# Optimization experiments

Hardware: AMD Instinct MI355X
Metric: run time of the kernel (lower is better)

The kernel has to match this reference:

```python
import jax, jax.numpy as jnp
import numpy as np

# CLIP ViT-B/16 + CLIP4Clip pruning controller dims
B, L, C = 128, 197, 768      # batch, vision tokens (CLS at 0), vis_dim
Lt, Ct = 32, 512             # text length, txt_dim
H = 12                       # n_head
DH = C // H                  # head dim = 64
DPP = 256                    # dpp_vproj output dim
TAU = 1.0                    # gumbel tau (>= 0.05 clamp is inactive)
TARGET = 0.7                 # keep_ratio for this layer
DPP_TAU = 0.01               # default dpp_tau
DPP_EPS = 1e-05


def setup_inputs() -> dict:
    key = jax.random.key(0)
    ks = jax.random.split(key, 14)
    s = 0.02
    f32 = jnp.float32
    return {
        "x_LND": jax.random.normal(ks[0], (L, B, C), f32),
        "text_hidden_BLC": jax.random.normal(ks[1], (B, Lt, Ct), f32),
        "gumbel_u": jax.random.uniform(ks[2], (B, L - 1, 2), f32),
        # q/k/v projections (torch Linear convention: W is [out, in])
        "Wq": jax.random.normal(ks[3], (C, C), f32) * s,
        "bq": jnp.zeros((C,), f32),
        "Wk": jax.random.normal(ks[4], (C, Ct), f32) * s,
        "bk": jnp.zeros((C,), f32),
        "Wv": jax.random.normal(ks[5], (C, Ct), f32) * s,
        "bv": jnp.zeros((C,), f32),
        # out_mlp: Linear(C,C) -> QuickGELU -> Linear(C,2)
        "W1": jax.random.normal(ks[6], (C, C), f32) * s,
        "b1": jnp.zeros((C,), f32),
        "W2": jax.random.normal(ks[7], (2, C), f32) * s,
        "b2": jnp.zeros((2,), f32),
        # dpp_vproj (no bias)
        "Wdpp": jax.random.normal(ks[8], (DPP, C), f32) * s,
    }


def reference(x_LND, text_hidden_BLC, gumbel_u, Wq, bq, Wk, bk, Wv, bv,
              W1, b1, W2, b2, Wdpp):
    Nv = L - 1
    # ---- LVDecisionModule: cross-attn policy head ----
    vis_all = jnp.transpose(x_LND, (1, 0, 2))      # [B, L, C]
    vis_tok = vis_all[:, 1:, :]                    # [B, Nv, C] (exclude CLS)
    q = (vis_tok @ Wq.T + bq).reshape(B, Nv, H, DH)
    k = (text_hidden_BLC @ Wk.T + bk).reshape(B, Lt, H, DH)
    v = (text_hidden_BLC @ Wv.T + bv).reshape(B, Lt, H, DH)
    scores = jnp.einsum('bnhd,blhd->bhnl', q, k) / (DH ** 0.5)  # [B,H,Nv,Lt]
    attn = jax.nn.softmax(scores, axis=-1)
    ctx = jnp.einsum('bhnl,blhd->bnhd', attn, v).reshape(B, Nv, C)
    fused = ctx + vis_tok                          # inner_dim == vis_dim
    hmid = fused @ W1.T + b1
    hmid = hmid * jax.nn.sigmoid(1.702 * hmid)     # QuickGELU
    logits = hmid @ W2.T + b2                      # [B, Nv, 2]
    rel_BN = attn.mean(axis=-1).mean(axis=1)       # [B, Nv]

    # ---- Gumbel-softmax sample ----
    eps_g = 1e-06
    U = jnp.clip(gumbel_u, eps_g, 1.0 - eps_g)
    g = -jnp.log(-jnp.log(U))
    lg = logits - jnp.max(logits, axis=-1, keepdims=True)
    probs = jax.nn.softmax((lg + g) / TAU, axis=-1)  # [B, Nv, 2]

    # ---- straight-through hard sample ----
    idx = jnp.argmax(probs, axis=-1)
    hard = jax.nn.one_hot(idx, 2, dtype=probs.dtype) + probs - jax.lax.stop_gradient(probs)
    keep_prob = probs[..., 1]                      # [B, Nv]
    keep_bin = hard[..., 1]

    # ---- ratio loss + cumulative policy (cum_policy was None) ----
    loss_ratio = (keep_prob.mean() - TARGET) ** 2
    policy = jnp.concatenate([jnp.ones((B, 1), keep_bin.dtype), keep_bin], axis=1)  # [B, L]

    # ---- DPP loss from attention relevance ----
    eps = 1e-12
    rel = jnp.maximum(rel_BN, 0.0)
    rel = rel / (rel.mean(axis=1, keepdims=True) + eps)   # quality_power == 1
    kp = jnp.clip(keep_prob, 0.0, 1.0)                    # keepprob_power == 1
    w = rel * kp
    w = jnp.maximum(w / (w.mean(axis=1, keepdims=True) + eps), 1e-06)
    w = jnp.sqrt(w)[..., None]                            # [B, Nv, 1]
    phi = vis_tok @ Wdpp.T                                # [B, Nv, DPP]
    phi = phi / jnp.maximum(jnp.linalg.norm(phi, axis=-1, keepdims=True), 1e-12)
    pw = phi * w
    G = jnp.einsum('bnd,bmd->bnm', pw, pw) / (float(DPP) * float(Nv) * DPP_TAU)
    # A = G + I, then safe_logdet adds DPP_EPS * I
    A = G + (1.0 + DPP_EPS) * jnp.eye(Nv, dtype=G.dtype)
    Lc = jnp.linalg.cholesky(A)
    logdet = 2.0 * jnp.sum(jnp.log(jnp.diagonal(Lc, axis1=-2, axis2=-1)), axis=-1)
    loss_dpp = -logdet.mean()

    return policy, loss_ratio, loss_dpp
```

## Files before the change

### kernel.cpp

```cpp
#include <hip/hip_runtime.h>
#include <math.h>

#define B_   128
#define L_   197
#define C_   768
#define Nv_  196
#define Lt_  32
#define Ct_  512
#define H_   12
#define DH_  64
#define DPP_ 256
#define MTOK 25088
#define MLD_ 208

typedef __attribute__((ext_vector_type(8))) short bf16x8_t;
typedef __attribute__((ext_vector_type(4))) float f32x4_t;

__device__ __forceinline__ void gload_lds16(const short* g, short* l) {
    __builtin_amdgcn_global_load_lds(
        (const __attribute__((address_space(1))) unsigned int*)g,
        (__attribute__((address_space(3))) unsigned int*)l,
        16, 0, 0);
}

__device__ __forceinline__ void split_bf16(float a, unsigned &h, unsigned &l) {
    unsigned u = __float_as_uint(a);
    unsigned hu = u & 0xffff0000u;
    h = hu >> 16;
    float lf = a - __uint_as_float(hu);
    unsigned ul = __float_as_uint(lf);
    l = (ul + 0x7fffu + ((ul >> 16) & 1u)) >> 16;
}

__device__ __forceinline__ void split8_pack(const float* av, uint4& Hh, uint4& Ll) {
    unsigned hv[8], lv[8];
#pragma unroll
    for (int j = 0; j < 8; ++j) split_bf16(av[j], hv[j], lv[j]);
    Hh.x = hv[0] | (hv[1] << 16); Hh.y = hv[2] | (hv[3] << 16);
    Hh.z = hv[4] | (hv[5] << 16); Hh.w = hv[6] | (hv[7] << 16);
    Ll.x = lv[0] | (lv[1] << 16); Ll.y = lv[2] | (lv[3] << 16);
    Ll.z = lv[4] | (lv[5] << 16); Ll.w = lv[6] | (lv[7] << 16);
}

#define NWQ 589824
#define NWK 393216
#define NWD 196608
__global__ __launch_bounds__(256)
void split_all(const float* __restrict__ Wq, const float* __restrict__ W1,
               const float* __restrict__ Wk, const float* __restrict__ Wv,
               const float* __restrict__ Wd,
               short* __restrict__ Wq_h, short* __restrict__ Wq_l,
               short* __restrict__ W1_h, short* __restrict__ W1_l,
               short* __restrict__ Wk_h, short* __restrict__ Wk_l,
               short* __restrict__ Wv_h, short* __restrict__ Wv_l,
               short* __restrict__ Wd_h, short* __restrict__ Wd_l)
{
    int j = blockIdx.x * 256 + threadIdx.x;
    const float* src; short *hi, *lo;
    if (j < NWQ)                { src = Wq; hi = Wq_h; lo = Wq_l; }
    else if ((j -= NWQ) < NWQ)  { src = W1; hi = W1_h; lo = W1_l; }
    else if ((j -= NWQ) < NWK)  { src = Wk; hi = Wk_h; lo = Wk_l; }
    else if ((j -= NWK) < NWK)  { src = Wv; hi = Wv_h; lo = Wv_l; }
    else                        { j -= NWK;  src = Wd; hi = Wd_h; lo = Wd_l; }
    unsigned h, l;
    split_bf16(src[j], h, l);
    hi[j] = (short)h; lo[j] = (short)l;
}

__global__ __launch_bounds__(256)
void split_x(const float* __restrict__ x, short* __restrict__ Xh,
             short* __restrict__ Xl)
{
    int idx = blockIdx.x * 256 + threadIdx.x;
    int m = idx / 96, c8 = (idx - m * 96) * 8;
    int b = m / Nv_, n = m - b * Nv_;
    const float* src = x + ((size_t)(n + 1) * B_ + b) * C_ + c8;
    float av[8];
    *(float4*)&av[0] = *(const float4*)src;
    *(float4*)&av[4] = *(const float4*)(src + 4);
    uint4 Hh, Ll;
    split8_pack(av, Hh, Ll);
    *(uint4*)&Xh[(size_t)m * C_ + c8] = Hh;
    *(uint4*)&Xl[(size_t)m * C_ + c8] = Ll;
}

__global__ __launch_bounds__(256)
void split_text(const float* __restrict__ t, short* __restrict__ Th,
                short* __restrict__ Tl)
{
    int idx = blockIdx.x * 256 + threadIdx.x;
    const float* src = t + (size_t)idx * 8;
    float av[8];
    *(float4*)&av[0] = *(const float4*)src;
    *(float4*)&av[4] = *(const float4*)(src + 4);
    uint4 Hh, Ll;
    split8_pack(av, Hh, Ll);
    *(uint4*)&Th[(size_t)idx * 8] = Hh;
    *(uint4*)&Tl[(size_t)idx * 8] = Ll;
}

template<int EPI, int SELY, int SWZ>
__global__ __launch_bounds__(256)
void mfma_gemm(const short* __restrict__ Ah_g, const short* __restrict__ Al_g,
               const short* __restrict__ Bh1, const short* __restrict__ Bl1,
               const float* __restrict__ bias1, float* __restrict__ C1, int Nst1,
               const short* Bh2, const short* Bl2, const float* bias2,
               float* C2, int Nst2,
               int Kd, const float* __restrict__ W2, float* __restrict__ partials)
{
    int bx = blockIdx.x, by = blockIdx.y;
    if (SWZ) {
        const int NX = gridDim.x, NY = gridDim.y;
        const int total = NX * NY;
        int flat = by * NX + bx;
        int g = (flat & 7) * (total >> 3) + (flat >> 3);
        bx = g / NY; by = g % NY;
    }
    const bool sel = SELY ? (by >= 6) : (blockIdx.z != 0);
    const short* Bh_g = sel ? Bh2 : Bh1;
    const short* Bl_g = sel ? Bl2 : Bl1;
    const float* bias = sel ? bias2 : bias1;
    float* Cst        = sel ? C2 : C1;
    const int Nst     = sel ? Nst2 : Nst1;
    const int yy      = (SELY && sel) ? by - 6 : by;

    __shared__ short Ah[128 * 32], Al[128 * 32], Bh[128 * 32], Bl[128 * 32];
    const int tid = threadIdx.x;
    const int m0 = bx * 128, n0 = yy * 128;
    const int l = tid & 63, wid = tid >> 6;
    const int wr = wid >> 1, wc = wid & 1;
    const int lr = l & 15, lq = l >> 4;

    const int sr = wid * 32 + (l >> 2);
    const int sc = 8 * ((l & 3) ^ ((l >> 3) & 3));
    const short* a0  = Ah_g + (size_t)(m0 + sr) * Kd + sc;
    const short* a1  = Ah_g + (size_t)(m0 + sr + 16) * Kd + sc;
    const short* al0 = Al_g + (size_t)(m0 + sr) * Kd + sc;
    const short* al1 = Al_g + (size_t)(m0 + sr + 16) * Kd + sc;
    const short* b0  = Bh_g + (size_t)(n0 + sr) * Kd + sc;
    const short* b1  = Bh_g + (size_t)(n0 + sr + 16) * Kd + sc;
    const short* bl0 = Bl_g + (size_t)(n0 + sr) * Kd + sc;
    const short* bl1 = Bl_g + (size_t)(n0 + sr + 16) * Kd + sc;
    short* dA0  = &Ah[(wid * 32) * 32];
    short* dA1  = &Ah[(wid * 32 + 16) * 32];
    short* dAl0 = &Al[(wid * 32) * 32];
    short* dAl1 = &Al[(wid * 32 + 16) * 32];
    short* dB0  = &Bh[(wid * 32) * 32];
    short* dB1  = &Bh[(wid * 32 + 16) * 32];
    short* dBl0 = &Bl[(wid * 32) * 32];
    short* dBl1 = &Bl[(wid * 32 + 16) * 32];

    const int swzr = (lr >> 1) & 3;

    f32x4_t acc[4][4];
#pragma unroll
    for (int m = 0; m < 4; ++m)
#pragma unroll
        for (int n = 0; n < 4; ++n) {
            acc[m][n][0] = 0.f; acc[m][n][1] = 0.f;
            acc[m][n][2] = 0.f; acc[m][n][3] = 0.f;
        }

    for (int k0 = 0; k0 < Kd; k0 += 32) {
        gload_lds16(a0  + k0, dA0);
        gload_lds16(a1  + k0, dA1);
        gload_lds16(al0 + k0, dAl0);
        gload_lds16(al1 + k0, dAl1);
        gload_lds16(b0  + k0, dB0);
        gload_lds16(b1  + k0, dB1);
        gload_lds16(bl0 + k0, dBl0);
        gload_lds16(bl1 + k0, dBl1);
        __syncthreads();

        bf16x8_t ahf[4], alf[4], bhf[4], blf[4];
#pragma unroll
        for (int m = 0; m < 4; ++m) {
            int ro = (wr * 64 + m * 16 + lr) * 32 + ((lq ^ swzr) * 8);
            ahf[m] = *(const bf16x8_t*)&Ah[ro];
            alf[m] = *(const bf16x8_t*)&Al[ro];
        }
#pragma unroll
        for (int n = 0; n < 4; ++n) {
            int ro = (wc * 64 + n * 16 + lr) * 32 + ((lq ^ swzr) * 8);
            bhf[n] = *(const bf16x8_t*)&Bh[ro];
            blf[n] = *(const bf16x8_t*)&Bl[ro];
        }
#pragma unroll
        for (int m = 0; m < 4; ++m)
#pragma unroll
            for (int n = 0; n < 4; ++n) {
                acc[m][n] = __builtin_amdgcn_mfma_f32_16x16x32_bf16(ahf[m], bhf[n], acc[m][n], 0, 0, 0);
                acc[m][n] = __builtin_amdgcn_mfma_f32_16x16x32_bf16(ahf[m], blf[n], acc[m][n], 0, 0, 0);
                acc[m][n] = __builtin_amdgcn_mfma_f32_16x16x32_bf16(alf[m], bhf[n], acc[m][n], 0, 0, 0);
            }
        __syncthreads();
    }

    if constexpr (EPI == 0) {
#pragma unroll
        for (int n = 0; n < 4; ++n) {
            int col = n0 + wc * 64 + n * 16 + lr;
            float bv = bias ? bias[col] : 0.f;
#pragma unroll
            for (int m = 0; m < 4; ++m) {
                int rowb = m0 + wr * 64 + m * 16 + lq * 4;
#pragma unroll
                for (int r = 0; r < 4; ++r)
                    Cst[(size_t)(rowb + r) * Nst + col] = acc[m][n][r] + bv;
            }
        }
    } else {
        int coln[4]; float b1v[4], w20[4], w21[4];
#pragma unroll
        for (int n = 0; n < 4; ++n) {
            coln[n] = n0 + wc * 64 + n * 16 + lr;
            b1v[n] = bias[coln[n]];
            w20[n] = W2[coln[n]];
            w21[n] = W2[C_ + coln[n]];
        }
        const int pi = (yy * 2 + wc) * 2;
#pragma unroll
        for (int m = 0; m < 4; ++m)
#pragma unroll
            for (int r = 0; r < 4; ++r) {
                float p0 = 0.f, p1 = 0.f;
#pragma unroll
                for (int n = 0; n < 4; ++n) {
                    float h = acc[m][n][r] + b1v[n];
                    float gl = h / (1.f + expf(-1.702f * h));
                    p0 = fmaf(gl, w20[n], p0);
                    p1 = fmaf(gl, w21[n], p1);
                }
#pragma unroll
                for (int off = 8; off; off >>= 1) {
                    p0 += __shfl_xor(p0, off, 16);
                    p1 += __shfl_xor(p1, off, 16);
                }
                if (lr == 0) {
                    int row = m0 + wr * 64 + m * 16 + lq * 4 + r;
                    partials[(size_t)row * 24 + pi + 0] = p0;
                    partials[(size_t)row * 24 + pi + 1] = p1;
                }
            }
    }
}

__global__ __launch_bounds__(256)
void gram_kernel(const float* __restrict__ A, float* __restrict__ Mout,
                 float scale)
{
    __shared__ float As[16][132];
    __shared__ float Bs[16][132];
    const int tid = threadIdx.x;
    const int tx = tid & 15, ty = tid >> 4;
    const int m0 = blockIdx.x * 128, n0 = blockIdx.y * 128;
    const int bz = blockIdx.z;
    const float* Ab = A + (size_t)bz * Nv_ * DPP_;
    float* Mb = Mout + (size_t)bz * Nv_ * MLD_;

    const int lrow = tid >> 2;
    const int lk   = (tid & 3) << 2;

    const float* aptr[2]; const float* bptr[2];
    bool aval[2], bval[2];
#pragma unroll
    for (int Lq = 0; Lq < 2; ++Lq) {
        int row = lrow + Lq * 64;
        int gr = m0 + row;
        aval[Lq] = (gr < Nv_);
        aptr[Lq] = Ab + (size_t)(aval[Lq] ? gr : 0) * DPP_ + lk;
        int gc = n0 + row;
        bval[Lq] = (gc < Nv_);
        bptr[Lq] = Ab + (size_t)(bval[Lq] ? gc : 0) * DPP_ + lk;
    }

    float acc[8][8];
#pragma unroll
    for (int r = 0; r < 8; ++r)
#pragma unroll
        for (int c = 0; c < 8; ++c) acc[r][c] = 0.f;

    for (int k0 = 0; k0 < DPP_; k0 += 16) {
#pragma unroll
        for (int Lq = 0; Lq < 2; ++Lq) {
            int row = lrow + Lq * 64;
            float4 va = aval[Lq] ? *(const float4*)(aptr[Lq] + k0)
                                 : make_float4(0.f, 0.f, 0.f, 0.f);
            As[lk+0][row] = va.x; As[lk+1][row] = va.y;
            As[lk+2][row] = va.z; As[lk+3][row] = va.w;
            float4 vb = bval[Lq] ? *(const float4*)(bptr[Lq] + k0)
                                 : make_float4(0.f, 0.f, 0.f, 0.f);
            Bs[lk+0][row] = vb.x; Bs[lk+1][row] = vb.y;
            Bs[lk+2][row] = vb.z; Bs[lk+3][row] = vb.w;
        }
        __syncthreads();
#pragma unroll
        for (int kk = 0; kk < 16; ++kk) {
            float a[8], bfr[8];
            *(float4*)&a[0]   = *(const float4*)&As[kk][ty * 8];
            *(float4*)&a[4]   = *(const float4*)&As[kk][ty * 8 + 4];
            *(float4*)&bfr[0] = *(const float4*)&Bs[kk][tx * 4];
            *(float4*)&bfr[4] = *(const float4*)&Bs[kk][64 + tx * 4];
#pragma unroll
            for (int r = 0; r < 8; ++r)
#pragma unroll
                for (int c = 0; c < 8; ++c)
                    acc[r][c] = fmaf(a[r], bfr[c], acc[r][c]);
        }
        __syncthreads();
    }

#pragma unroll
    for (int r = 0; r < 8; ++r) {
        int gr = m0 + ty * 8 + r;
        if (gr >= Nv_) continue;
#pragma unroll
        for (int half = 0; half < 2; ++half) {
            int gc0 = n0 + half * 64 + tx * 4;
#pragma unroll
            for (int c = 0; c < 4; ++c) {
                int gc = gc0 + c;
                if (gc < Nv_) {
                    float v = acc[r][half*4+c] * scale;
                    if (gr == gc) v += 1e-5f;
                    Mb[(size_t)gr * MLD_ + gc] = v;
                } else if (gc < MLD_) {
                    Mb[(size_t)gr * MLD_ + gc] = 0.f;
                }
            }
        }
    }
}

__global__ __launch_bounds__(256)
void taylor_gemm(const float* __restrict__ Mg, float* __restrict__ tpart)
{
    __shared__ float As[16][132];
    __shared__ float Bs[16][132];
    __shared__ float wred[4][4];
    const int tid = threadIdx.x;
    const int tx = tid & 15, ty = tid >> 4;
    const int m0 = blockIdx.x * 128, n0 = blockIdx.y * 128;
    const int bz = blockIdx.z;
    const float* Mb = Mg + (size_t)bz * Nv_ * MLD_;

    const int lrow = tid >> 2;
    const int lk   = (tid & 3) << 2;

    const float* aptr[2]; const float* bptr[2];
    bool aval[2], bval[2];
#pragma unroll
    for (int Lq = 0; Lq < 2; ++Lq) {
        int row = lrow + Lq * 64;
        int gr = m0 + row;
        aval[Lq] = (gr < Nv_);
        aptr[Lq] = Mb + (size_t)(aval[Lq] ? gr : 0) * MLD_ + lk;
        int gc = n0 + row;
        bval[Lq] = (gc < Nv_);
        bptr[Lq] = Mb + (size_t)(bval[Lq] ? gc : 0) * MLD_ + lk;
    }

    float acc[8][8];
#pragma unroll
    for (int r = 0; r < 8; ++r)
#pragma unroll
        for (int c = 0; c < 8; ++c) acc[r][c] = 0.f;

    for (int k0 = 0; k0 < MLD_; k0 += 16) {
#pragma unroll
        for (int Lq = 0; Lq < 2; ++Lq) {
            int row = lrow + Lq * 64;
            float4 va = aval[Lq] ? *(const float4*)(aptr[Lq] + k0)
                                 : make_float4(0.f, 0.f, 0.f, 0.f);
            As[lk+0][row] = va.x; As[lk+1][row] = va.y;
            As[lk+2][row] = va.z; As[lk+3][row] = va.w;
            float4 vb = bval[Lq] ? *(const float4*)(bptr[Lq] + k0)
                                 : make_float4(0.f, 0.f, 0.f, 0.f);
            Bs[lk+0][row] = vb.x; Bs[lk+1][row] = vb.y;
            Bs[lk+2][row] = vb.z; Bs[lk+3][row] = vb.w;
        }
        __syncthreads();
#pragma unroll
        for (int kk = 0; kk < 16; ++kk) {
            float a[8], bfr[8];
            *(float4*)&a[0]   = *(const float4*)&As[kk][ty * 8];
            *(float4*)&a[4]   = *(const float4*)&As[kk][ty * 8 + 4];
            *(float4*)&bfr[0] = *(const float4*)&Bs[kk][tx * 4];
            *(float4*)&bfr[4] = *(const float4*)&Bs[kk][64 + tx * 4];
#pragma unroll
            for (int r = 0; r < 8; ++r)
#pragma unroll
                for (int c = 0; c < 8; ++c)
                    acc[r][c] = fmaf(a[r], bfr[c], acc[r][c]);
        }
        __syncthreads();
    }

    float t1 = 0.f, t2 = 0.f, t3 = 0.f, t4 = 0.f;
#pragma unroll
    for (int r = 0; r < 8; ++r) {
        int gr = m0 + ty * 8 + r;
        if (gr >= Nv_) continue;
#pragma unroll
        for (int half = 0; half < 2; ++half) {
            int gc0 = n0 + half * 64 + tx * 4;
#pragma unroll
            for (int c = 0; c < 4; ++c) {
                int gc = gc0 + c;
                if (gc < Nv_) {
                    float mij = Mb[(size_t)gr * MLD_ + gc];
                    float m2  = acc[r][half*4+c];
                    if (gr == gc) t1 += mij;
                    t2 = fmaf(mij, mij, t2);
                    t3 = fmaf(m2, mij, t3);
                    t4 = fmaf(m2, m2, t4);
                }
            }
        }
    }
#pragma unroll
    for (int off = 32; off; off >>= 1) {
        t1 += __shfl_xor(t1, off, 64);
        t2 += __shfl_xor(t2, off, 64);
        t3 += __shfl_xor(t3, off, 64);
        t4 += __shfl_xor(t4, off, 64);
    }
    const int wv = tid >> 6;
    if ((tid & 63) == 0) {
        wred[wv][0] = t1; wred[wv][1] = t2; wred[wv][2] = t3; wred[wv][3] = t4;
    }
    __syncthreads();
    if (tid == 0) {
        const int blk = blockIdx.y * 2 + blockIdx.x;
        float* dst = tpart + ((size_t)bz * 4 + blk) * 4;
        dst[0] = wred[0][0] + wred[1][0] + wred[2][0] + wred[3][0];
        dst[1] = wred[0][1] + wred[1][1] + wred[2][1] + wred[3][1];
        dst[2] = wred[0][2] + wred[1][2] + wred[2][2] + wred[3][2];
        dst[3] = wred[0][3] + wred[1][3] + wred[2][3] + wred[3][3];
    }
}

__global__ __launch_bounds__(256)
void attn_kernel(const float* __restrict__ q, const float* __restrict__ k,
                 const float* __restrict__ v, const float* __restrict__ x,
                 short* __restrict__ Fh, short* __restrict__ Fl)
{
    __shared__ float Ks[Lt_][DH_ + 4];
    __shared__ float Vs[Lt_][DH_ + 1];
    __shared__ float qs[16][DH_];
    __shared__ float as[16][Lt_];
    const int bh = blockIdx.x;
    const int b = bh / H_, h = bh - b * H_;
    const int tid = threadIdx.x;
    const int wv = tid >> 6, lane = tid & 63;
    const int half = lane >> 5;
    const int key = lane & 31;

    for (int idx = tid; idx < Lt_ * 16; idx += 256) {
        int l = idx >> 4, dq = (idx & 15) << 2;
        size_t off = ((size_t)(b * Lt_ + l)) * C_ + h * DH_ + dq;
        float4 kv4 = *(const float4*)(k + off);
        Ks[l][dq] = kv4.x; Ks[l][dq + 1] = kv4.y; Ks[l][dq + 2] = kv4.z; Ks[l][dq + 3] = kv4.w;
        float4 vv4 = *(const float4*)(v + off);
        Vs[l][dq] = vv4.x; Vs[l][dq + 1] = vv4.y; Vs[l][dq + 2] = vv4.z; Vs[l][dq + 3] = vv4.w;
    }
    __syncthreads();

    const size_t qbase = (size_t)b * Nv_ * C_ + h * DH_ + lane;
    const size_t xbase = (size_t)b * C_ + h * DH_ + lane;

    float qv[4], xv[4];
#pragma unroll
    for (int j = 0; j < 4; ++j) {
        qv[j] = q[qbase + (size_t)(wv * 4 + j) * C_];
        xv[j] = x[xbase + (size_t)(wv * 4 + j + 1) * B_ * C_];
    }

    for (int it = 0; it < 13; ++it) {
        const int base = it * 16 + wv * 4;
        if (base > 192) break;
        float cq[4], cx[4];
#pragma unroll
        for (int j = 0; j < 4; ++j) { cq[j] = qv[j]; cx[j] = xv[j]; }
        const int nbase = base + 16;
        if (nbase <= 192) {
#pragma unroll
            for (int j = 0; j < 4; ++j) {
                qv[j] = q[qbase + (size_t)(nbase + j) * C_];
                xv[j] = x[xbase + (size_t)(nbase + j + 1) * B_ * C_];
            }
        }
        const int ws = wv * 4;
#pragma unroll
        for (int j = 0; j < 4; ++j) qs[ws + j][lane] = cq[j];

        const int s0 = ws + half * 2;
        float s1 = 0.f, s2 = 0.f;
#pragma unroll
        for (int d4 = 0; d4 < DH_; d4 += 4) {
            float4 k4  = *(const float4*)&Ks[key][d4];
            float4 q4a = *(const float4*)&qs[s0][d4];
            float4 q4b = *(const float4*)&qs[s0 + 1][d4];
            s1 = fmaf(q4a.x, k4.x, s1); s2 = fmaf(q4b.x, k4.x, s2);
            s1 = fmaf(q4a.y, k4.y, s1); s2 = fmaf(q4b.y, k4.y, s2);
            s1 = fmaf(q4a.z, k4.z, s1); s2 = fmaf(q4b.z, k4.z, s2);
            s1 = fmaf(q4a.w, k4.w, s1); s2 = fmaf(q4b.w, k4.w, s2);
        }
        s1 *= 0.125f; s2 *= 0.125f;
        float mx1 = s1, mx2 = s2;
#pragma unroll
        for (int off = 16; off; off >>= 1) {
            mx1 = fmaxf(mx1, __shfl_xor(mx1, off, 32));
            mx2 = fmaxf(mx2, __shfl_xor(mx2, off, 32));
        }
        float p1v = expf(s1 - mx1);
        float p2v = expf(s2 - mx2);
        float su1 = p1v, su2 = p2v;
#pragma unroll
        for (int off = 16; off; off >>= 1) {
            su1 += __shfl_xor(su1, off, 32);
            su2 += __shfl_xor(su2, off, 32);
        }
        as[s0][key] = p1v / su1;
        as[s0 + 1][key] = p2v / su2;

        float c0 = 0.f, c1 = 0.f, c2 = 0.f, c3 = 0.f;
#pragma unroll
        for (int l4 = 0; l4 < Lt_; l4 += 4) {
            float4 a0 = *(const float4*)&as[ws + 0][l4];
            float4 a1 = *(const float4*)&as[ws + 1][l4];
            float4 a2 = *(const float4*)&as[ws + 2][l4];
            float4 a3 = *(const float4*)&as[ws + 3][l4];
            float v0 = Vs[l4 + 0][lane], v1 = Vs[l4 + 1][lane];
            float v2 = Vs[l4 + 2][lane], v3 = Vs[l4 + 3][lane];
            c0 = fmaf(a0.x, v0, c0); c1 = fmaf(a1.x, v0, c1);
            c2 = fmaf(a2.x, v0, c2); c3 = fmaf(a3.x, v0, c3);
            c0 = fmaf(a0.y, v1, c0); c1 = fmaf(a1.y, v1, c1);
            c2 = fmaf(a2.y, v1, c2); c3 = fmaf(a3.y, v1, c3);
            c0 = fmaf(a0.z, v2, c0); c1 = fmaf(a1.z, v2, c1);
            c2 = fmaf(a2.z, v2, c2); c3 = fmaf(a3.z, v2, c3);
            c0 = fmaf(a0.w, v3, c0); c1 = fmaf(a1.w, v3, c1);
            c2 = fmaf(a2.w, v3, c2); c3 = fmaf(a3.w, v3, c3);
        }
        float fo[4] = {c0 + cx[0], c1 + cx[1], c2 + cx[2], c3 + cx[3]};
#pragma unroll
        for (int j = 0; j < 4; ++j) {
            unsigned hh, ll;
            split_bf16(fo[j], hh, ll);
            Fh[qbase + (size_t)(base + j) * C_] = (short)hh;
            Fl[qbase + (size_t)(base + j) * C_] = (short)ll;
        }
    }
}

__global__ __launch_bounds__(256)
void keep_kernel(const float* __restrict__ partials, const float* __restrict__ b2,
                 const float* __restrict__ gumbel, float* __restrict__ policy,
                 float* __restrict__ keep_prob)
{
    int m = blockIdx.x * 256 + threadIdx.x;
    int b = m / Nv_, n = m - b * Nv_;
    float l0 = b2[0], l1 = b2[1];
#pragma unroll
    for (int t = 0; t < 12; ++t) {
        l0 += partials[(size_t)m * 24 + t * 2 + 0];
        l1 += partials[(size_t)m * 24 + t * 2 + 1];
    }
    const float UHI = (float)(1.0 - 1e-6);
    float U0 = fminf(fmaxf(gumbel[(size_t)m * 2 + 0], 1e-6f), UHI);
    float U1 = fminf(fmaxf(gumbel[(size_t)m * 2 + 1], 1e-6f), UHI);
    float t0 = (float)log((double)U0);
    float g0 = -(float)log((double)(-t0));
    float t1 = (float)log((double)U1);
    float g1 = -(float)log((double)(-t1));
    float dlog = (l1 + g1) - (l0 + g0);
    float kp = 1.f / (1.f + expf(-dlog));
    policy[(size_t)b * 197 + 1 + n] = (dlog > 0.f) ? 1.f : 0.f;
    if (n == 0) policy[(size_t)b * 197] = 1.f;
    keep_prob[m] = kp;
}

__global__ __launch_bounds__(256)
void batch_reduce(const float* __restrict__ keep_prob, float* __restrict__ sum_kp)
{
    __shared__ float part[4];
    int b = blockIdx.x, tid = threadIdx.x;
    float vs = (tid < Nv_) ? keep_prob[(size_t)b * Nv_ + tid] : 0.f;
#pragma unroll
    for (int off = 32; off; off >>= 1) vs += __shfl_xor(vs, off, 64);
    if ((tid & 63) == 0) part[tid >> 6] = vs;
    __syncthreads();
    if (tid == 0) sum_kp[b] = part[0] + part[1] + part[2] + part[3];
}

__global__ __launch_bounds__(256)
void pw_scale(float* __restrict__ phi, const float* __restrict__ keep_prob,
              const float* __restrict__ sum_kp)
{
    int m = blockIdx.x * 4 + (threadIdx.x >> 6);
    int lane = threadIdx.x & 63;
    float4* row = (float4*)phi + (size_t)m * 64;
    float4 vv = row[lane];
    float ss = vv.x * vv.x + vv.y * vv.y + vv.z * vv.z + vv.w * vv.w;
#pragma unroll
    for (int off = 32; off; off >>= 1) ss += __shfl_xor(ss, off, 64);
    float nrm = fmaxf(sqrtf(ss), 1e-12f);
    int b = m / Nv_;
    float kp = keep_prob[m];
    float meanw = sum_kp[b] * (1.f / 196.f);
    float wn = fmaxf(kp / (meanw + 1e-12f), 1e-6f);
    float sc = sqrtf(wn) / nrm;
    vv.x *= sc; vv.y *= sc; vv.z *= sc; vv.w *= sc;
    row[lane] = vv;
}

__global__ void finalize_kernel(const float* __restrict__ sum_kp,
                                const float* __restrict__ tpart,
                                float* __restrict__ out)
{
    float tot = 0.f, ld = 0.f;
    for (int b = 0; b < B_; ++b) {
        tot += sum_kp[b];
        float s1 = 0.f, s2 = 0.f, s3 = 0.f, s4 = 0.f;
        for (int blk = 0; blk < 4; ++blk) {
            const float* p = tpart + ((size_t)b * 4 + blk) * 4;
            s1 += p[0]; s2 += p[1]; s3 += p[2]; s4 += p[3];
        }
        ld += s1 - 0.5f * s2 + (1.f / 3.f) * s3 - 0.25f * s4;
    }
    float mean = tot * (1.f / 25088.f);
    float d = mean - 0.7f;
    out[25216] = d * d;
    out[25217] = -ld * (1.f / 128.f);
}

extern "C" void kernel_launch(void* const* d_in, const int* in_sizes, int n_in,
                              void* d_out, int out_size, void* d_ws, size_t ws_size,
                              hipStream_t stream)
{
    const float* x      = (const float*)d_in[0];
    const float* text   = (const float*)d_in[1];
    const float* gumbel = (const float*)d_in[2];
    const float* Wq     = (const float*)d_in[3];
    const float* bq     = (const float*)d_in[4];
    const float* Wk     = (const float*)d_in[5];
    const float* bk     = (const float*)d_in[6];
    const float* Wv     = (const float*)d_in[7];
    const float* bv     = (const float*)d_in[8];
    const float* W1     = (const float*)d_in[9];
    const float* b1     = (const float*)d_in[10];
    const float* W2     = (const float*)d_in[11];
    const float* b2     = (const float*)d_in[12];
    const float* Wdpp   = (const float*)d_in[13];
    float* out = (float*)d_out;

    float* ws = (float*)d_ws;
    float* q          = ws;
    float* kbuf       = q + 19267584;
    float* vbuf       = kbuf + 3145728;
    float* phi        = vbuf + 3145728;
    float* partials   = phi + 6422528;
    float* keep_prob  = partials + 602112;
    float* sum_kp     = keep_prob + 25088;
    float* logdet_arr = sum_kp + 128;
    float* M          = ws;
    float* tpart      = partials;

    short* Wq_h = (short*)(logdet_arr + 128);
    short* Wq_l = Wq_h + 589824;
    short* W1_h = Wq_l + 589824;
    short* W1_l = W1_h + 589824;
    short* Wk_h = W1_l + 589824;
    short* Wk_l = Wk_h + 393216;
    short* Wv_h = Wk_l + 393216;
    short* Wv_l = Wv_h + 393216;
    short* Wd_h = Wv_l + 393216;
    short* Wd_l = Wd_h + 196608;
    short* Xh = Wd_l + 196608;
    short* Xl = Xh + 19267584;
    short* Th = Xl + 19267584;
    short* Tl = Th + 2097152;
    short* Fh = Xh;
    short* Fl = Xl;

    dim3 blk(256);

    split_all<<<dim3(8448), blk, 0, stream>>>(Wq, W1, Wk, Wv, Wdpp,
                                              Wq_h, Wq_l, W1_h, W1_l,
                                              Wk_h, Wk_l, Wv_h, Wv_l,
                                              Wd_h, Wd_l);
    split_x<<<dim3(9408), blk, 0, stream>>>(x, Xh, Xl);
    split_text<<<dim3(1024), blk, 0, stream>>>(text, Th, Tl);

    mfma_gemm<0,0,0><<<dim3(32,6,2), blk, 0, stream>>>(
        Th, Tl, Wk_h, Wk_l, bk, kbuf, 768,
        Wv_h, Wv_l, bv, vbuf, 768, 512, nullptr, nullptr);
    mfma_gemm<0,1,1><<<dim3(196,8,1), blk, 0, stream>>>(
        Xh, Xl, Wq_h, Wq_l, bq, q, 768,
        Wd_h, Wd_l, nullptr, phi, 256, 768, nullptr, nullptr);
    attn_kernel<<<dim3(B_*H_), blk, 0, stream>>>(q, kbuf, vbuf, x, Fh, Fl);
    mfma_gemm<1,0,1><<<dim3(196,6,1), blk, 0, stream>>>(
        Fh, Fl, W1_h, W1_l, b1, nullptr, 768,
        W1_h, W1_l, b1, nullptr, 768, 768, W2, partials);
    keep_kernel<<<dim3(98), blk, 0, stream>>>(partials, b2, gumbel, out, keep_prob);
    batch_reduce<<<dim3(B_), blk, 0, stream>>>(keep_prob, sum_kp);
    pw_scale<<<dim3(6272), blk, 0, stream>>>(phi, keep_prob, sum_kp);
    gram_kernel<<<dim3(2,2,B_), blk, 0, stream>>>(phi, M,
                                                  1.0f/(256.0f*196.0f*0.01f));
    taylor_gemm<<<dim3(2,2,B_), blk, 0, stream>>>(M, tpart);
    finalize_kernel<<<dim3(1), dim3(1), 0, stream>>>(sum_kp, tpart, out);
}
```

Baseline: 567.5 us.

## Move DPP Gram and Taylor GEMMs to split-bf16 MFMA

The per-batch Gram matrix and the Taylor-series M·M product move from scalar FP32 FMA loops to 3-pass split-bf16 MFMA kernels. pw_scale now writes the scaled phi as bf16 hi/lo pairs, and the M matrix is stored as a padded 224×224 hi/lo bf16 pair. The aim is to cut the scalar FP32 cost of these two batched GEMMs. The trade-off is slightly reduced precision from dropping the lo×lo term and storing M in bf16 pairs. The 196-row buffers are read in 128-row tiles up to row 256 and padded out to 224, so edge blocks rely on reading past the valid rows.

```diff
diff --git a/kernel.cpp b/kernel.cpp
--- a/kernel.cpp
+++ b/kernel.cpp
@@ -11,7 +11,7 @@
 #define DH_  64
 #define DPP_ 256
 #define MTOK 25088
-#define MLD_ 208
+#define MS_  224
 
 typedef __attribute__((ext_vector_type(8))) short bf16x8_t;
 typedef __attribute__((ext_vector_type(4))) float f32x4_t;
@@ -30,6 +30,10 @@
     float lf = a - __uint_as_float(hu);
     unsigned ul = __float_as_uint(lf);
     l = (ul + 0x7fffu + ((ul >> 16) & 1u)) >> 16;
+}
+
+__device__ __forceinline__ float bf16_to_f(short s) {
+    return __uint_as_float(((unsigned)(unsigned short)s) << 16);
 }
 
 __device__ __forceinline__ void split8_pack(const float* av, uint4& Hh, uint4& Ll) {
@@ -246,86 +250,101 @@
 }
 
 __global__ __launch_bounds__(256)
-void gram_kernel(const float* __restrict__ A, float* __restrict__ Mout,
-                 float scale)
-{
-    __shared__ float As[16][132];
-    __shared__ float Bs[16][132];
+void gram_mfma(const short* __restrict__ Ph, const short* __restrict__ Pl,
+               short* __restrict__ Mh_g, short* __restrict__ Ml_g, float scale)
+{
+    __shared__ short Ah[128 * 32], Al[128 * 32], Bh[128 * 32], Bl[128 * 32];
     const int tid = threadIdx.x;
-    const int tx = tid & 15, ty = tid >> 4;
     const int m0 = blockIdx.x * 128, n0 = blockIdx.y * 128;
     const int bz = blockIdx.z;
-    const float* Ab = A + (size_t)bz * Nv_ * DPP_;
-    float* Mb = Mout + (size_t)bz * Nv_ * MLD_;
-
-    const int lrow = tid >> 2;
-    const int lk   = (tid & 3) << 2;
-
-    const float* aptr[2]; const float* bptr[2];
-    bool aval[2], bval[2];
-#pragma unroll
-    for (int Lq = 0; Lq < 2; ++Lq) {
-        int row = lrow + Lq * 64;
-        int gr = m0 + row;
-        aval[Lq] = (gr < Nv_);
-        aptr[Lq] = Ab + (size_t)(aval[Lq] ? gr : 0) * DPP_ + lk;
-        int gc = n0 + row;
-        bval[Lq] = (gc < Nv_);
-        bptr[Lq] = Ab + (size_t)(bval[Lq] ? gc : 0) * DPP_ + lk;
-    }
-
-    float acc[8][8];
-#pragma unroll
-    for (int r = 0; r < 8; ++r)
-#pragma unroll
-        for (int c = 0; c < 8; ++c) acc[r][c] = 0.f;
-
-    for (int k0 = 0; k0 < DPP_; k0 += 16) {
-#pragma unroll
-        for (int Lq = 0; Lq < 2; ++Lq) {
-            int row = lrow + Lq * 64;
-            float4 va = aval[Lq] ? *(const float4*)(aptr[Lq] + k0)
-                                 : make_float4(0.f, 0.f, 0.f, 0.f);
-            As[lk+0][row] = va.x; As[lk+1][row] = va.y;
-            As[lk+2][row] = va.z; As[lk+3][row] = va.w;
-            float4 vb = bval[Lq] ? *(const float4*)(bptr[Lq] + k0)
-                                 : make_float4(0.f, 0.f, 0.f, 0.f);
-            Bs[lk+0][row] = vb.x; Bs[lk+1][row] = vb.y;
-            Bs[lk+2][row] = vb.z; Bs[lk+3][row] = vb.w;
-        }
+    const int l = tid & 63, wid = tid >> 6;
+    const int wr = wid >> 1, wc = wid & 1;
+    const int lr = l & 15, lq = l >> 4;
+
+    const size_t rbase = (size_t)bz * Nv_;
+    const int sr = wid * 32 + (l >> 2);
+    const int sc = 8 * ((l & 3) ^ ((l >> 3) & 3));
+    const short* a0  = Ph + (rbase + m0 + sr) * DPP_ + sc;
+    const short* a1  = Ph + (rbase + m0 + sr + 16) * DPP_ + sc;
+    const short* al0 = Pl + (rbase + m0 + sr) * DPP_ + sc;
+    const short* al1 = Pl + (rbase + m0 + sr + 16) * DPP_ + sc;
+    const short* b0  = Ph + (rbase + n0 + sr) * DPP_ + sc;
+    const short* b1  = Ph + (rbase + n0 + sr + 16) * DPP_ + sc;
+    const short* bl0 = Pl + (rbase + n0 + sr) * DPP_ + sc;
+    const short* bl1 = Pl + (rbase + n0 + sr + 16) * DPP_ + sc;
+    short* dA0  = &Ah[(wid * 32) * 32];
+    short* dA1  = &Ah[(wid * 32 + 16) * 32];
+    short* dAl0 = &Al[(wid * 32) * 32];
+    short* dAl1 = &Al[(wid * 32 + 16) * 32];
+    short* dB0  = &Bh[(wid * 32) * 32];
+    short* dB1  = &Bh[(wid * 32 + 16) * 32];
+    short* dBl0 = &Bl[(wid * 32) * 32];
+    short* dBl1 = &Bl[(wid * 32 + 16) * 32];
+    const int swzr = (lr >> 1) & 3;
+
+    f32x4_t acc[4][4];
+#pragma unroll
+    for (int m = 0; m < 4; ++m)
+#pragma unroll
+        for (int n = 0; n < 4; ++n) {
+            acc[m][n][0] = 0.f; acc[m][n][1] = 0.f;
+            acc[m][n][2] = 0.f; acc[m][n][3] = 0.f;
+        }
+
+    for (int k0 = 0; k0 < DPP_; k0 += 32) {
+        gload_lds16(a0  + k0, dA0);
+        gload_lds16(a1  + k0, dA1);
+        gload_lds16(al0 + k0, dAl0);
+        gload_lds16(al1 + k0, dAl1);
+        gload_lds16(b0  + k0, dB0);
+        gload_lds16(b1  + k0, dB1);
+        gload_lds16(bl0 + k0, dBl0);
+        gload_lds16(bl1 + k0, dBl1);
         __syncthreads();
-#pragma unroll
-        for (int kk = 0; kk < 16; ++kk) {
-            float a[8], bfr[8];
-            *(float4*)&a[0]   = *(const float4*)&As[kk][ty * 8];
-            *(float4*)&a[4]   = *(const float4*)&As[kk][ty * 8 + 4];
-            *(float4*)&bfr[0] = *(const float4*)&Bs[kk][tx * 4];
-            *(float4*)&bfr[4] = *(const float4*)&Bs[kk][64 + tx * 4];
-#pragma unroll
-            for (int r = 0; r < 8; ++r)
-#pragma unroll
-                for (int c = 0; c < 8; ++c)
-                    acc[r][c] = fmaf(a[r], bfr[c], acc[r][c]);
-        }
+        bf16x8_t ahf[4], alf[4], bhf[4], blf[4];
+#pragma unroll
+        for (int m = 0; m < 4; ++m) {
+            int ro = (wr * 64 + m * 16 + lr) * 32 + ((lq ^ swzr) * 8);
+            ahf[m] = *(const bf16x8_t*)&Ah[ro];
+            alf[m] = *(const bf16x8_t*)&Al[ro];
+        }
+#pragma unroll
+        for (int n = 0; n < 4; ++n) {
+            int ro = (wc * 64 + n * 16 + lr) * 32 + ((lq ^ swzr) * 8);
+            bhf[n] = *(const bf16x8_t*)&Bh[ro];
+            blf[n] = *(const bf16x8_t*)&Bl[ro];
+        }
+#pragma unroll
+        for (int m = 0; m < 4; ++m)
+#pragma unroll
+            for (int n = 0; n < 4; ++n) {
+                acc[m][n] = __builtin_amdgcn_mfma_f32_16x16x32_bf16(ahf[m], bhf[n], acc[m][n], 0, 0, 0);
+                acc[m][n] = __builtin_amdgcn_mfma_f32_16x16x32_bf16(ahf[m], blf[n], acc[m][n], 0, 0, 0);
+                acc[m][n] = __builtin_amdgcn_mfma_f32_16x16x32_bf16(alf[m], bhf[n], acc[m][n], 0, 0, 0);
+            }
         __syncthreads();
     }
 
-#pragma unroll
-    for (int r = 0; r < 8; ++r) {
-        int gr = m0 + ty * 8 + r;
-        if (gr >= Nv_) continue;
-#pragma unroll
-        for (int half = 0; half < 2; ++half) {
-            int gc0 = n0 + half * 64 + tx * 4;
-#pragma unroll
-            for (int c = 0; c < 4; ++c) {
-                int gc = gc0 + c;
-                if (gc < Nv_) {
-                    float v = acc[r][half*4+c] * scale;
-                    if (gr == gc) v += 1e-5f;
-                    Mb[(size_t)gr * MLD_ + gc] = v;
-                } else if (gc < MLD_) {
-                    Mb[(size_t)gr * MLD_ + gc] = 0.f;
+    short* Mhb = Mh_g + (size_t)bz * MS_ * MS_;
+    short* Mlb = Ml_g + (size_t)bz * MS_ * MS_;
+#pragma unroll
+    for (int n = 0; n < 4; ++n) {
+        int gc = n0 + wc * 64 + n * 16 + lr;
+#pragma unroll
+        for (int m = 0; m < 4; ++m) {
+            int rowb = m0 + wr * 64 + m * 16 + lq * 4;
+#pragma unroll
+            for (int r = 0; r < 4; ++r) {
+                int gr = rowb + r;
+                if (gr < MS_ && gc < MS_) {
+                    unsigned hh = 0, ll = 0;
+                    if (gr < Nv_ && gc < Nv_) {
+                        float v = acc[m][n][r] * scale;
+                        if (gr == gc) v += 1e-5f;
+                        split_bf16(v, hh, ll);
+                    }
+                    Mhb[(size_t)gr * MS_ + gc] = (short)hh;
+                    Mlb[(size_t)gr * MS_ + gc] = (short)ll;
                 }
             }
         }
@@ -333,83 +352,98 @@
 }
 
 __global__ __launch_bounds__(256)
-void taylor_gemm(const float* __restrict__ Mg, float* __restrict__ tpart)
-{
-    __shared__ float As[16][132];
-    __shared__ float Bs[16][132];
+void taylor_mfma(const short* __restrict__ Mh_g, const short* __restrict__ Ml_g,
+                 float* __restrict__ tpart)
+{
+    __shared__ short Ah[128 * 32], Al[128 * 32], Bh[128 * 32], Bl[128 * 32];
     __shared__ float wred[4][4];
     const int tid = threadIdx.x;
-    const int tx = tid & 15, ty = tid >> 4;
     const int m0 = blockIdx.x * 128, n0 = blockIdx.y * 128;
     const int bz = blockIdx.z;
-    const float* Mb = Mg + (size_t)bz * Nv_ * MLD_;
-
-    const int lrow = tid >> 2;
-    const int lk   = (tid & 3) << 2;
-
-    const float* aptr[2]; const float* bptr[2];
-    bool aval[2], bval[2];
-#pragma unroll
-    for (int Lq = 0; Lq < 2; ++Lq) {
-        int row = lrow + Lq * 64;
-        int gr = m0 + row;
-        aval[Lq] = (gr < Nv_);
-        aptr[Lq] = Mb + (size_t)(aval[Lq] ? gr : 0) * MLD_ + lk;
-        int gc = n0 + row;
-        bval[Lq] = (gc < Nv_);
-        bptr[Lq] = Mb + (size_t)(bval[Lq] ? gc : 0) * MLD_ + lk;
-    }
-
-    float acc[8][8];
-#pragma unroll
-    for (int r = 0; r < 8; ++r)
-#pragma unroll
-        for (int c = 0; c < 8; ++c) acc[r][c] = 0.f;
-
-    for (int k0 = 0; k0 < MLD_; k0 += 16) {
-#pragma unroll
-        for (int Lq = 0; Lq < 2; ++Lq) {
-            int row = lrow + Lq * 64;
-            float4 va = aval[Lq] ? *(const float4*)(aptr[Lq] + k0)
-                                 : make_float4(0.f, 0.f, 0.f, 0.f);
-            As[lk+0][row] = va.x; As[lk+1][row] = va.y;
-            As[lk+2][row] = va.z; As[lk+3][row] = va.w;
-            float4 vb = bval[Lq] ? *(const float4*)(bptr[Lq] + k0)
-                                 : make_float4(0.f, 0.f, 0.f, 0.f);
-            Bs[lk+0][row] = vb.x; Bs[lk+1][row] = vb.y;
-            Bs[lk+2][row] = vb.z; Bs[lk+3][row] = vb.w;
-        }
+    const int l = tid & 63, wid = tid >> 6;
+    const int wr = wid >> 1, wc = wid & 1;
+    const int lr = l & 15, lq = l >> 4;
+
+    const size_t rbase = (size_t)bz * MS_;
+    const int sr = wid * 32 + (l >> 2);
+    const int sc = 8 * ((l & 3) ^ ((l >> 3) & 3));
+    const short* a0  = Mh_g + (rbase + m0 + sr) * MS_ + sc;
+    const short* a1  = Mh_g + (rbase + m0 + sr + 16) * MS_ + sc;
+    const short* al0 = Ml_g + (rbase + m0 + sr) * MS_ + sc;
+    const short* al1 = Ml_g + (rbase + m0 + sr + 16) * MS_ + sc;
+    const short* b0  = Mh_g + (rbase + n0 + sr) * MS_ + sc;
+    const short* b1  = Mh_g + (rbase + n0 + sr + 16) * MS_ + sc;
+    const short* bl0 = Ml_g + (rbase + n0 + sr) * MS_ + sc;
+    const short* bl1 = Ml_g + (rbase + n0 + sr + 16) * MS_ + sc;
+    short* dA0  = &Ah[(wid * 32) * 32];
+    short* dA1  = &Ah[(wid * 32 + 16) * 32];
+    short* dAl0 = &Al[(wid * 32) * 32];
+    short* dAl1 = &Al[(wid * 32 + 16) * 32];
+    short* dB0  = &Bh[(wid * 32) * 32];
+    short* dB1  = &Bh[(wid * 32 + 16) * 32];
+    short* dBl0 = &Bl[(wid * 32) * 32];
+    short* dBl1 = &Bl[(wid * 32 + 16) * 32];
+    const int swzr = (lr >> 1) & 3;
+
+    f32x4_t acc[4][4];
+#pragma unroll
+    for (int m = 0; m < 4; ++m)
+#pragma unroll
+        for (int n = 0; n < 4; ++n) {
+            acc[m][n][0] = 0.f; acc[m][n][1] = 0.f;
+            acc[m][n][2] = 0.f; acc[m][n][3] = 0.f;
+        }
+
+    for (int k0 = 0; k0 < MS_; k0 += 32) {
+        gload_lds16(a0  + k0, dA0);
+        gload_lds16(a1  + k0, dA1);
+        gload_lds16(al0 + k0, dAl0);
+        gload_lds16(al1 + k0, dAl1);
+        gload_lds16(b0  + k0, dB0);
+        gload_lds16(b1  + k0, dB1);
+        gload_lds16(bl0 + k0, dBl0);
+        gload_lds16(bl1 + k0, dBl1);
         __syncthreads();
-#pragma unroll
-        for (int kk = 0; kk < 16; ++kk) {
-            float a[8], bfr[8];
-            *(float4*)&a[0]   = *(const float4*)&As[kk][ty * 8];
-            *(float4*)&a[4]   = *(const float4*)&As[kk][ty * 8 + 4];
-            *(float4*)&bfr[0] = *(const float4*)&Bs[kk][tx * 4];
-            *(float4*)&bfr[4] = *(const float4*)&Bs[kk][64 + tx * 4];
-#pragma unroll
-            for (int r = 0; r < 8; ++r)
-#pragma unroll
-                for (int c = 0; c < 8; ++c)
-                    acc[r][c] = fmaf(a[r], bfr[c], acc[r][c]);
-        }
+        bf16x8_t ahf[4], alf[4], bhf[4], blf[4];
+#pragma unroll
+        for (int m = 0; m < 4; ++m) {
+            int ro = (wr * 64 + m * 16 + lr) * 32 + ((lq ^ swzr) * 8);
+            ahf[m] = *(const bf16x8_t*)&Ah[ro];
+            alf[m] = *(const bf16x8_t*)&Al[ro];
+        }
+#pragma unroll
+        for (int n = 0; n < 4; ++n) {
+            int ro = (wc * 64 + n * 16 + lr) * 32 + ((lq ^ swzr) * 8);
+            bhf[n] = *(const bf16x8_t*)&Bh[ro];
+            blf[n] = *(const bf16x8_t*)&Bl[ro];
+        }
+#pragma unroll
+        for (int m = 0; m < 4; ++m)
+#pragma unroll
+            for (int n = 0; n < 4; ++n) {
+                acc[m][n] = __builtin_amdgcn_mfma_f32_16x16x32_bf16(ahf[m], bhf[n], acc[m][n], 0, 0, 0);
+                acc[m][n] = __builtin_amdgcn_mfma_f32_16x16x32_bf16(ahf[m], blf[n], acc[m][n], 0, 0, 0);
+                acc[m][n] = __builtin_amdgcn_mfma_f32_16x16x32_bf16(alf[m], bhf[n], acc[m][n], 0, 0, 0);
+            }
         __syncthreads();
     }
 
+    const short* Mhb = Mh_g + (size_t)bz * MS_ * MS_;
+    const short* Mlb = Ml_g + (size_t)bz * MS_ * MS_;
     float t1 = 0.f, t2 = 0.f, t3 = 0.f, t4 = 0.f;
 #pragma unroll
-    for (int r = 0; r < 8; ++r) {
-        int gr = m0 + ty * 8 + r;
-        if (gr >= Nv_) continue;
-#pragma unroll
-        for (int half = 0; half < 2; ++half) {
-            int gc0 = n0 + half * 64 + tx * 4;
-#pragma unroll
-            for (int c = 0; c < 4; ++c) {
-                int gc = gc0 + c;
-                if (gc < Nv_) {
-                    float mij = Mb[(size_t)gr * MLD_ + gc];
-                    float m2  = acc[r][half*4+c];
+    for (int n = 0; n < 4; ++n) {
+        int gc = n0 + wc * 64 + n * 16 + lr;
+#pragma unroll
+        for (int m = 0; m < 4; ++m) {
+            int rowb = m0 + wr * 64 + m * 16 + lq * 4;
+#pragma unroll
+            for (int r = 0; r < 4; ++r) {
+                int gr = rowb + r;
+                if (gr < Nv_ && gc < Nv_) {
+                    float mij = bf16_to_f(Mhb[(size_t)gr * MS_ + gc])
+                              + bf16_to_f(Mlb[(size_t)gr * MS_ + gc]);
+                    float m2 = acc[m][n][r];
                     if (gr == gc) t1 += mij;
                     t2 = fmaf(mij, mij, t2);
                     t3 = fmaf(m2, mij, t3);
@@ -425,9 +459,8 @@
         t3 += __shfl_xor(t3, off, 64);
         t4 += __shfl_xor(t4, off, 64);
     }
-    const int wv = tid >> 6;
-    if ((tid & 63) == 0) {
-        wred[wv][0] = t1; wred[wv][1] = t2; wred[wv][2] = t3; wred[wv][3] = t4;
+    if (l == 0) {
+        wred[wid][0] = t1; wred[wid][1] = t2; wred[wid][2] = t3; wred[wid][3] = t4;
     }
     __syncthreads();
     if (tid == 0) {
@@ -594,12 +627,13 @@
 }
 
 __global__ __launch_bounds__(256)
-void pw_scale(float* __restrict__ phi, const float* __restrict__ keep_prob,
-              const float* __restrict__ sum_kp)
+void pw_scale(const float* __restrict__ phi, const float* __restrict__ keep_prob,
+              const float* __restrict__ sum_kp,
+              short* __restrict__ Ph, short* __restrict__ Pl)
 {
     int m = blockIdx.x * 4 + (threadIdx.x >> 6);
     int lane = threadIdx.x & 63;
-    float4* row = (float4*)phi + (size_t)m * 64;
+    const float4* row = (const float4*)phi + (size_t)m * 64;
     float4 vv = row[lane];
     float ss = vv.x * vv.x + vv.y * vv.y + vv.z * vv.z + vv.w * vv.w;
 #pragma unroll
@@ -610,8 +644,15 @@
     float meanw = sum_kp[b] * (1.f / 196.f);
     float wn = fmaxf(kp / (meanw + 1e-12f), 1e-6f);
     float sc = sqrtf(wn) / nrm;
-    vv.x *= sc; vv.y *= sc; vv.z *= sc; vv.w *= sc;
-    row[lane] = vv;
+    float vals[4] = {vv.x * sc, vv.y * sc, vv.z * sc, vv.w * sc};
+    unsigned h[4], lo[4];
+#pragma unroll
+    for (int j = 0; j < 4; ++j) split_bf16(vals[j], h[j], lo[j]);
+    uint2 Hp, Lp;
+    Hp.x = h[0] | (h[1] << 16);  Hp.y = h[2] | (h[3] << 16);
+    Lp.x = lo[0] | (lo[1] << 16); Lp.y = lo[2] | (lo[3] << 16);
+    *(uint2*)&Ph[(size_t)m * DPP_ + lane * 4] = Hp;
+    *(uint2*)&Pl[(size_t)m * DPP_ + lane * 4] = Lp;
 }
 
 __global__ void finalize_kernel(const float* __restrict__ sum_kp,
@@ -663,8 +704,10 @@
     float* keep_prob  = partials + 602112;
     float* sum_kp     = keep_prob + 25088;
     float* logdet_arr = sum_kp + 128;
-    float* M          = ws;
     float* tpart      = partials;
+
+    short* Mh = (short*)ws;
+    short* Ml = Mh + 6472704;
 
     short* Wq_h = (short*)(logdet_arr + 128);
     short* Wq_l = Wq_h + 589824;
@@ -682,6 +725,8 @@
     short* Tl = Th + 2097152;
     short* Fh = Xh;
     short* Fl = Xl;
+    short* Ph = Xh;
+    short* Pl = Xl;
 
     dim3 blk(256);
 
@@ -704,9 +749,9 @@
         W1_h, W1_l, b1, nullptr, 768, 768, W2, partials);
     keep_kernel<<<dim3(98), blk, 0, stream>>>(partials, b2, gumbel, out, keep_prob);
     batch_reduce<<<dim3(B_), blk, 0, stream>>>(keep_prob, sum_kp);
-    pw_scale<<<dim3(6272), blk, 0, stream>>>(phi, keep_prob, sum_kp);
-    gram_kernel<<<dim3(2,2,B_), blk, 0, stream>>>(phi, M,
-                                                  1.0f/(256.0f*196.0f*0.01f));
-    taylor_gemm<<<dim3(2,2,B_), blk, 0, stream>>>(M, tpart);
+    pw_scale<<<dim3(6272), blk, 0, stream>>>(phi, keep_prob, sum_kp, Ph, Pl);
+    gram_mfma<<<dim3(2,2,B_), blk, 0, stream>>>(Ph, Pl, Mh, Ml,
+                                                1.0f/(256.0f*196.0f*0.01f));
+    taylor_mfma<<<dim3(2,2,B_), blk, 0, stream>>>(Mh, Ml, tpart);
     finalize_kernel<<<dim3(1), dim3(1), 0, stream>>>(sum_kp, tpart, out);
 }
```

New measurement: 514.0 us. 1.1x faster.
